# Performance work log

Measured on AMD Instinct MI355X. Metric: run time of the kernel, lower is better.

## Reference

```python
import jax, jax.numpy as jnp
import numpy as np

EPS = 1e-5

def bn_lastdim(x, g, b):
    # BatchNorm2d (training-mode batch stats) applied over all axes except last channel axis
    m = x.mean(axis=(0, 1, 2), keepdims=True)
    v = x.var(axis=(0, 1, 2), keepdims=True)
    return g * (x - m) * jax.lax.rsqrt(v + EPS) + b

def setup_inputs() -> dict:
    key = jax.random.key(0)
    ks = jax.random.split(key, 8)
    B, N, M, F1, K = 8, 8192, 2048, 64, 32
    PF, OUT, DIV = 64, 128, 4
    IN_CH = PF + F1  # 128
    inp = {
        "points": jax.random.normal(ks[0], (B, N, 3), jnp.float32),
        "queries": jax.random.normal(ks[1], (B, M, 3), jnp.float32),
        "feat_prev": jax.random.normal(ks[2], (B, N, F1), jnp.float32),
        # Lift params: linear1 3->32, linear2 32->64
        "w1": jax.random.normal(ks[3], (3, PF // 2), jnp.float32) * 0.1,
        "b1": jnp.zeros((PF // 2,), jnp.float32),
        "w2": jax.random.normal(ks[4], (PF // 2, PF), jnp.float32) * 0.1,
        "b2": jnp.zeros((PF,), jnp.float32),
        # batchnorm affine params (bn1 over 3, bn2 over 32, bn3 over in_channel)
        "g1": jnp.ones((3,), jnp.float32), "be1": jnp.zeros((3,), jnp.float32),
        "g2": jnp.ones((PF // 2,), jnp.float32), "be2": jnp.zeros((PF // 2,), jnp.float32),
        "g3": jnp.ones((IN_CH,), jnp.float32), "be3": jnp.zeros((IN_CH,), jnp.float32),
        # conv2d (out, in, 1, division) -> drop singleton H dim
        "wc": jax.random.normal(ks[5], (OUT, IN_CH, DIV), jnp.float32) * 0.05,
        "bc": jnp.zeros((OUT,), jnp.float32),
    }
    return inp

def reference(points, queries, feat_prev, w1, b1, w2, b2, g1, be1, g2, be2, g3, be3, wc, bc):
    K = 32
    DIV = 4
    S = K // DIV  # maxpool window/stride along neighbor axis
    B = points.shape[0]

    # ---- KNN: squared distances (same ordering as torch.cdist + topk smallest) ----
    pn = jnp.sum(points * points, axis=-1)   # (B,N)
    qn = jnp.sum(queries * queries, axis=-1) # (B,M)
    d2 = qn[:, :, None] + pn[:, None, :] - 2.0 * jnp.einsum('bmd,bnd->bmn', queries, points)
    _, idx = jax.lax.top_k(-d2, K)           # idx: (B,M,K), sorted nearest-first

    batch_ix = jnp.arange(B)[:, None, None]
    knn_pts = points[batch_ix, idx]          # (B,M,K,3)
    local = queries[:, :, None, :] - knn_pts # (B,M,K,3)

    # ---- Lift MLP (with batchnorm, training-mode stats) ----
    h = bn_lastdim(local, g1, be1)
    h = jax.nn.relu(h @ w1 + b1)             # (B,M,K,32)
    h = bn_lastdim(h, g2, be2)
    h = jax.nn.relu(h @ w2 + b2)             # (B,M,K,64)

    # ---- gather previous features, concat ----
    knn_prev = feat_prev[batch_ix, idx]      # (B,M,K,F1)
    feat = jnp.concatenate([h, knn_prev], axis=-1)  # (B,M,K,C) C=128

    # ---- maxpool over neighbor axis (window S, stride S) ----
    Bq, M, _, C = feat.shape
    feat = feat.reshape(Bq, M, DIV, S, C).max(axis=3)  # (B,M,DIV,C)

    # ---- BN + conv2d kernel (1,DIV) + relu; width collapses to 1 ----
    feat = bn_lastdim(feat, g3, be3)
    out = jnp.einsum('bmdc,ocd->bmo', feat, wc) + bc
    return jax.nn.relu(out)                  # (B,M,out_features)
```

## Files before the change

kernel.cpp:

```cpp
#include <hip/hip_runtime.h>
#include <math.h>

#define B_   8
#define N_   8192
#define M_   2048
#define KNN  32
#define F1_  64
#define HID  32
#define DIV_ 4

typedef unsigned long long u64;
typedef unsigned int u32;

__global__ __launch_bounds__(256) void pack_kernel(
    const float* __restrict__ points, float4* __restrict__ ppk)
{
  const int i = blockIdx.x*256 + threadIdx.x;
  const float* pp = &points[(size_t)i*3];
  float px = pp[0], py = pp[1], pz = pp[2];
  float pn = __builtin_fmaf(pz, pz, __builtin_fmaf(py, py, __fmul_rn(px, px)));
  ppk[i] = make_float4(px, py, pz, pn);
}

__device__ __forceinline__ u32 ord_f32(float f) {
  u32 u = __float_as_uint(f);
  return u ^ (u32)(((int)u >> 31) | 0x80000000);
}

#define KNN_INSERT(PV, NV)                                                    \
  {                                                                           \
    const u32 n_ = (NV);                                                      \
    _Pragma("unroll")                                                         \
    for (int q = 0; q < 2; ++q) {                                             \
      float dot = __builtin_fmaf(qz[q], (PV).z,                               \
                  __builtin_fmaf(qy[q], (PV).y, __fmul_rn(qx[q], (PV).x)));   \
      float s_  = __fadd_rn(qn[q], (PV).w);                                   \
      float d2  = __builtin_fmaf(-2.0f, dot, s_);                             \
      const bool lt0 = d2 < c0[q];                                            \
      const bool lt1 = d2 < c1[q];                                            \
      const bool lt2 = d2 < c2[q];                                            \
      c2[q] = lt1 ? c1[q] : (lt2 ? d2 : c2[q]);                               \
      i2[q] = lt1 ? i1[q] : (lt2 ? n_ : i2[q]);                               \
      c1[q] = lt0 ? c0[q] : (lt1 ? d2 : c1[q]);                               \
      i1[q] = lt0 ? i0[q] : (lt1 ? n_ : i1[q]);                               \
      c0[q] = lt0 ? d2 : c0[q];                                               \
      i0[q] = lt0 ? n_ : i0[q];                                               \
    }                                                                         \
  }

__global__ __launch_bounds__(256, 6) void knn_kernel(
    const float4* __restrict__ ppk, const float* __restrict__ queries,
    int* __restrict__ idx_out, float* __restrict__ local_out)
{
  const int bid = blockIdx.x;
  const int b = bid >> 8;
  const int qbase = (bid & 255) * 8;
  const int t = threadIdx.x, lane = t & 63, wid = t >> 6;

  const int q0 = qbase + wid*2;
  float qx[2], qy[2], qz[2], qn[2];
  float c0[2], c1[2], c2[2];
  u32 i0[2], i1[2], i2[2];
  #pragma unroll
  for (int q = 0; q < 2; ++q) {
    int m = q0 + q;
    qx[q] = queries[(b*M_+m)*3+0];
    qy[q] = queries[(b*M_+m)*3+1];
    qz[q] = queries[(b*M_+m)*3+2];
    qn[q] = __builtin_fmaf(qz[q], qz[q], __builtin_fmaf(qy[q], qy[q], __fmul_rn(qx[q], qx[q])));
    c0[q] = c1[q] = c2[q] = __builtin_inff();
    i0[q] = i1[q] = i2[q] = 0u;
  }

  const float4* __restrict__ base = ppk + (size_t)b * N_;

  float4 pa = base[lane];
  float4 pb = base[64 + lane];
  #pragma unroll 2
  for (int j = 0; j < 126; ++j) {
    const float4 pc = base[(j+2)*64 + lane];
    KNN_INSERT(pa, j*64 + lane);
    pa = pb; pb = pc;
  }
  KNN_INSERT(pa, 126*64 + lane);
  KNN_INSERT(pb, 127*64 + lane);

  u64 e0[2], e1[2], e2[2];
  #pragma unroll
  for (int q = 0; q < 2; ++q) {
    e0[q] = ((u64)ord_f32(c0[q]) << 32) | i0[q];
    e1[q] = ((u64)ord_f32(c1[q]) << 32) | i1[q];
    e2[q] = ((u64)ord_f32(c2[q]) << 32) | i2[q];
  }
  u64 cand[2] = {e0[0], e0[1]};
  u64 mykey[2] = {~0ull, ~0ull};
  int rem[2] = {3, 3};

  for (int r = 0; r < KNN; ++r) {
    u64 wa = cand[0], wb = cand[1];
    #pragma unroll
    for (int dlt = 1; dlt < 64; dlt <<= 1) {
      u64 oa = __shfl_xor(wa, dlt);
      u64 ob = __shfl_xor(wb, dlt);
      wa = oa < wa ? oa : wa;
      wb = ob < wb ? ob : wb;
    }
    if (lane == r) { mykey[0] = wa; mykey[1] = wb; }
    u64 w2q[2] = {wa, wb};
    #pragma unroll
    for (int q = 0; q < 2; ++q) {
      const u64 w = w2q[q];
      if (cand[q] == w) {
        e0[q] = e1[q]; e1[q] = e2[q]; e2[q] = ~0ull; --rem[q];
        if (rem[q] == 0) {
          const u64 lim = w;
          u64 f0 = ~0ull, f1 = ~0ull, f2 = ~0ull;
          for (int j = 0; j < 128; ++j) {
            int n = j*64 + lane;
            const float4 p = base[n];
            float dot = __builtin_fmaf(qz[q], p.z, __builtin_fmaf(qy[q], p.y, __fmul_rn(qx[q], p.x)));
            float d2  = __builtin_fmaf(-2.0f, dot, __fadd_rn(qn[q], p.w));
            u64 key = ((u64)ord_f32(d2) << 32) | (u32)n;
            if (key > lim) {
              u64 a0 = key < f0 ? key : f0;
              u64 A0 = key < f0 ? f0  : key;
              u64 a1 = A0 < f1 ? A0   : f1;
              u64 A1 = A0 < f1 ? f1   : A0;
              u64 a2 = A1 < f2 ? A1   : f2;
              f0 = a0; f1 = a1; f2 = a2;
            }
          }
          e0[q] = f0; e1[q] = f1; e2[q] = f2;
          rem[q] = (f2 != ~0ull) ? 3 : ((f1 != ~0ull) ? 2 : ((f0 != ~0ull) ? 1 : 0));
        }
        cand[q] = e0[q];
      }
    }
  }

  #pragma unroll
  for (int q = 0; q < 2; ++q) {
    if (lane < KNN) {
      u32 n = (u32)mykey[q];
      int bm = b*M_ + q0 + q;
      idx_out[bm*KNN + lane] = (int)n;
      const float4 p = base[n];
      local_out[(bm*KNN + lane)*3 + 0] = qx[q] - p.x;
      local_out[(bm*KNN + lane)*3 + 1] = qy[q] - p.y;
      local_out[(bm*KNN + lane)*3 + 2] = qz[q] - p.z;
    }
  }
}

__global__ __launch_bounds__(256) void bn1_stats_kernel(
    const float* __restrict__ local, float* __restrict__ p1)
{
  const int t = threadIdx.x;
  const int gid = blockIdx.x*256 + t;
  float s0=0,s1=0,s2=0,q0=0,q1=0,q2=0;
  for (int r = gid; r < B_*M_*KNN; r += 65536) {
    float a = local[r*3+0], b = local[r*3+1], c = local[r*3+2];
    s0 += a; s1 += b; s2 += c;
    q0 = fmaf(a,a,q0); q1 = fmaf(b,b,q1); q2 = fmaf(c,c,q2);
  }
  __shared__ float red[256][8];
  red[t][0]=s0; red[t][1]=s1; red[t][2]=s2; red[t][3]=0.f;
  red[t][4]=q0; red[t][5]=q1; red[t][6]=q2; red[t][7]=0.f;
  __syncthreads();
  for (int st = 128; st >= 1; st >>= 1) {
    if (t < st) {
      #pragma unroll
      for (int j = 0; j < 8; ++j) red[t][j] += red[t+st][j];
    }
    __syncthreads();
  }
  if (t < 8) p1[blockIdx.x*8 + t] = red[0][t];
}

__global__ __launch_bounds__(128) void bn1_fold_kernel(
    const float* __restrict__ p1, const float* __restrict__ g1, const float* __restrict__ be1,
    const float* __restrict__ w1, const float* __restrict__ b1, float* __restrict__ prm)
{
  __shared__ float sc[3], sh[3];
  const int t = threadIdx.x;
  if (t < 3) {
    double s = 0, q = 0;
    for (int blk = 0; blk < 256; ++blk) { s += p1[blk*8+t]; q += p1[blk*8+4+t]; }
    double n = (double)(B_*M_*KNN);
    double m = s/n, v = q/n - m*m;
    double rs = 1.0/sqrt(v + 1e-5);
    float scale = (float)((double)g1[t]*rs);
    sc[t] = scale; sh[t] = be1[t] - (float)m*scale;
  }
  __syncthreads();
  if (t < 96) prm[t] = w1[t]*sc[t/32];
  if (t < 32) {
    float a = b1[t];
    for (int c = 0; c < 3; ++c) a = fmaf(sh[c], w1[c*32+t], a);
    prm[96+t] = a;
  }
}

__global__ __launch_bounds__(256) void h1_stats_kernel(
    const float* __restrict__ local, const float* __restrict__ prm, float* __restrict__ p2)
{
  const int t = threadIdx.x;
  const int k4 = (t & 7) * 4;
  float w0[4], w1q[4], w2q[4], b1q[4];
  #pragma unroll
  for (int i = 0; i < 4; ++i) {
    w0[i]  = prm[ 0 + k4 + i];
    w1q[i] = prm[32 + k4 + i];
    w2q[i] = prm[64 + k4 + i];
    b1q[i] = prm[96 + k4 + i];
  }
  float s[4] = {0,0,0,0}, sq[4] = {0,0,0,0};
  const int r0 = (blockIdx.x*256 + t) >> 3;
  for (int r = r0; r < B_*M_*KNN; r += 16384) {
    float l0 = local[r*3+0], l1 = local[r*3+1], l2 = local[r*3+2];
    #pragma unroll
    for (int i = 0; i < 4; ++i) {
      float v = fmaf(l2, w2q[i], fmaf(l1, w1q[i], fmaf(l0, w0[i], b1q[i])));
      v = fmaxf(v, 0.0f);
      s[i] += v; sq[i] = fmaf(v, v, sq[i]);
    }
  }
  __shared__ float red[256][8];
  #pragma unroll
  for (int i = 0; i < 4; ++i) { red[t][i] = s[i]; red[t][4+i] = sq[i]; }
  __syncthreads();
  for (int st = 128; st >= 8; st >>= 1) {
    if (t < st) {
      #pragma unroll
      for (int j = 0; j < 8; ++j) red[t][j] += red[t+st][j];
    }
    __syncthreads();
  }
  if (t < 8) {
    #pragma unroll
    for (int i = 0; i < 4; ++i) {
      p2[blockIdx.x*64 +      t*4 + i] = red[t][i];
      p2[blockIdx.x*64 + 32 + t*4 + i] = red[t][4+i];
    }
  }
}

__global__ __launch_bounds__(64) void bn2_fold_kernel(
    const float* __restrict__ p2, const float* __restrict__ g2, const float* __restrict__ be2,
    const float* __restrict__ w2, const float* __restrict__ b2, float* __restrict__ prm)
{
  __shared__ float sc[32], sh[32];
  const int t = threadIdx.x;
  if (t < 32) {
    double s = 0, q = 0;
    for (int blk = 0; blk < 512; ++blk) { s += p2[blk*64+t]; q += p2[blk*64+32+t]; }
    double n = (double)(B_*M_*KNN);
    double m = s/n, v = q/n - m*m;
    double rs = 1.0/sqrt(v + 1e-5);
    float scale = (float)((double)g2[t]*rs);
    sc[t] = scale; sh[t] = be2[t] - (float)m*scale;
  }
  __syncthreads();
  {
    int j = t;
    float a = b2[j];
    for (int k = 0; k < 32; ++k) {
      float wv = w2[k*64 + j];
      prm[128 + j*32 + k] = wv * sc[k];
      a = fmaf(sh[k], wv, a);
    }
    prm[2176 + j] = a;
  }
}

__global__ __launch_bounds__(256) void h2_prev_pool_kernel(
    const float* __restrict__ local, const float* __restrict__ prm,
    const float* __restrict__ feat_prev, const int* __restrict__ idx,
    float* __restrict__ pooled)
{
  const int t = threadIdx.x;
  const int row = blockIdx.x*256 + t;
  const int bm = row >> 5, s = row & 31, d = s >> 3;
  const float l0 = local[row*3+0], l1 = local[row*3+1], l2 = local[row*3+2];
  float h1v[32];
  #pragma unroll
  for (int k = 0; k < 32; ++k) {
    float v = fmaf(l2, prm[64+k], fmaf(l1, prm[32+k], fmaf(l0, prm[0+k], prm[96+k])));
    h1v[k] = fmaxf(v, 0.0f);
  }
  const float* __restrict__ w2t = prm + 128;
  const float* __restrict__ b2f = prm + 2176;
  #pragma unroll 4
  for (int j = 0; j < 64; ++j) {
    float acc = b2f[j];
    #pragma unroll
    for (int k = 0; k < 32; ++k) acc = fmaf(h1v[k], w2t[j*32+k], acc);
    acc = fmaxf(acc, 0.0f);
    acc = fmaxf(acc, __shfl_xor(acc, 1));
    acc = fmaxf(acc, __shfl_xor(acc, 2));
    acc = fmaxf(acc, __shfl_xor(acc, 4));
    if ((s & 7) == 0) pooled[(bm*4 + d)*128 + j] = acc;
  }
  const int bm0 = blockIdx.x * 8;
  #pragma unroll
  for (int it = 0; it < 8; ++it) {
    const int task = it*256 + t;
    const int bmL  = task >> 8;
    const int dd   = (task >> 6) & 3;
    const int ch   = task & 63;
    const int bmg  = bm0 + bmL;
    const int bb   = bmg >> 11;
    float pm = -3.402823466e+38f;
    #pragma unroll
    for (int s8 = 0; s8 < 8; ++s8) {
      int n = idx[bmg*KNN + dd*8 + s8];
      float v = feat_prev[((size_t)(bb*N_ + n))*64 + ch];
      pm = fmaxf(pm, v);
    }
    pooled[(size_t)(bmg*4 + dd)*128 + 64 + ch] = pm;
  }
}

__global__ __launch_bounds__(256) void bn3_stats_kernel(
    const float* __restrict__ pooled, float* __restrict__ p3)
{
  const int t = threadIdx.x, c = t & 127, rr = t >> 7;
  float s = 0, q = 0;
  for (int r = blockIdx.x*2 + rr; r < B_*M_*DIV_; r += 512) {
    float v = pooled[(size_t)r*128 + c];
    s += v; q = fmaf(v, v, q);
  }
  __shared__ float red[256][2];
  red[t][0] = s; red[t][1] = q;
  __syncthreads();
  if (t < 128) {
    p3[blockIdx.x*256 +       t] = red[t][0] + red[t+128][0];
    p3[blockIdx.x*256 + 128 + t] = red[t][1] + red[t+128][1];
  }
}

__global__ __launch_bounds__(256) void bn3_fold_kernel(
    const float* __restrict__ p3, const float* __restrict__ g3, const float* __restrict__ be3,
    const float* __restrict__ wc, const float* __restrict__ bc, float* __restrict__ prm)
{
  __shared__ float sc[128], sh[128];
  const int t = threadIdx.x;
  if (t < 128) {
    double s = 0, q = 0;
    for (int blk = 0; blk < 256; ++blk) { s += p3[blk*256+t]; q += p3[blk*256+128+t]; }
    double n = (double)(B_*M_*DIV_);
    double m = s/n, v = q/n - m*m;
    double rs = 1.0/sqrt(v + 1e-5);
    float scale = (float)((double)g3[t]*rs);
    sc[t] = scale; sh[t] = be3[t] - (float)m*scale;
  }
  __syncthreads();
  for (int e = t; e < 512*128; e += 256) {
    int i = e >> 7, o = e & 127, dd = i >> 7, cc = i & 127;
    prm[2240 + e] = wc[o*512 + cc*4 + dd] * sc[cc];
  }
  if (t < 128) {
    int o = t;
    float a = bc[o];
    for (int cc = 0; cc < 128; ++cc) {
      float hsum = 0;
      #pragma unroll
      for (int dd = 0; dd < 4; ++dd) hsum += wc[o*512 + cc*4 + dd];
      a = fmaf(sh[cc], hsum, a);
    }
    prm[67776 + o] = a;
  }
}

__global__ __launch_bounds__(256) void conv_gemm_kernel(
    const float* __restrict__ pooled, const float* __restrict__ prm,
    float* __restrict__ outp)
{
  const float* __restrict__ Bw  = prm + 2240;
  const float* __restrict__ bcf = prm + 67776;
  __shared__ float As[32][36];
  __shared__ float Bs[32][128];
  const int t = threadIdx.x;
  const int cg_ = t & 15, rg = t >> 4;
  const int rowbase = blockIdx.x * 32;
  float acc[2][8];
  #pragma unroll
  for (int i = 0; i < 2; ++i)
    #pragma unroll
    for (int j = 0; j < 8; ++j) acc[i][j] = 0.f;

  float bb[8];
  #pragma unroll
  for (int j = 0; j < 8; ++j) bb[j] = bcf[cg_*8 + j];

  for (int k0 = 0; k0 < 512; k0 += 32) {
    {
      int r = t >> 3, qd = t & 7;
      const float4 v = *(const float4*)&pooled[(size_t)(rowbase+r)*512 + k0 + qd*4];
      As[qd*4+0][r] = v.x; As[qd*4+1][r] = v.y; As[qd*4+2][r] = v.z; As[qd*4+3][r] = v.w;
    }
    #pragma unroll
    for (int i = 0; i < 4; ++i) {
      int li = t + i*256;
      int kk = li >> 5, c4 = (li & 31) * 4;
      *(float4*)&Bs[kk][c4] = *(const float4*)&Bw[(size_t)(k0+kk)*128 + c4];
    }
    __syncthreads();
    #pragma unroll 8
    for (int kk = 0; kk < 32; ++kk) {
      float a0 = As[kk][rg*2], a1 = As[kk][rg*2+1];
      float4 b0 = *(const float4*)&Bs[kk][cg_*8];
      float4 b1 = *(const float4*)&Bs[kk][cg_*8+4];
      float bv[8] = {b0.x, b0.y, b0.z, b0.w, b1.x, b1.y, b1.z, b1.w};
      #pragma unroll
      for (int j = 0; j < 8; ++j) {
        acc[0][j] = fmaf(a0, bv[j], acc[0][j]);
        acc[1][j] = fmaf(a1, bv[j], acc[1][j]);
      }
    }
    __syncthreads();
  }
  #pragma unroll
  for (int i = 0; i < 2; ++i) {
    int r = rowbase + rg*2 + i;
    float4 o0, o1;
    o0.x = fmaxf(acc[i][0] + bb[0], 0.f);
    o0.y = fmaxf(acc[i][1] + bb[1], 0.f);
    o0.z = fmaxf(acc[i][2] + bb[2], 0.f);
    o0.w = fmaxf(acc[i][3] + bb[3], 0.f);
    o1.x = fmaxf(acc[i][4] + bb[4], 0.f);
    o1.y = fmaxf(acc[i][5] + bb[5], 0.f);
    o1.z = fmaxf(acc[i][6] + bb[6], 0.f);
    o1.w = fmaxf(acc[i][7] + bb[7], 0.f);
    *(float4*)&outp[(size_t)r*128 + cg_*8    ] = o0;
    *(float4*)&outp[(size_t)r*128 + cg_*8 + 4] = o1;
  }
}

extern "C" void kernel_launch(void* const* d_in, const int* in_sizes, int n_in,
                              void* d_out, int out_size, void* d_ws, size_t ws_size,
                              hipStream_t stream)
{
  (void)in_sizes; (void)n_in; (void)out_size; (void)ws_size;
  const float* points    = (const float*)d_in[0];
  const float* queries   = (const float*)d_in[1];
  const float* feat_prev = (const float*)d_in[2];
  const float* w1  = (const float*)d_in[3];
  const float* b1  = (const float*)d_in[4];
  const float* w2  = (const float*)d_in[5];
  const float* b2  = (const float*)d_in[6];
  const float* g1  = (const float*)d_in[7];
  const float* be1 = (const float*)d_in[8];
  const float* g2  = (const float*)d_in[9];
  const float* be2 = (const float*)d_in[10];
  const float* g3  = (const float*)d_in[11];
  const float* be3 = (const float*)d_in[12];
  const float* wc  = (const float*)d_in[13];
  const float* bc  = (const float*)d_in[14];
  float* outp = (float*)d_out;

  char* ws = (char*)d_ws;
  int*   idx    = (int*)ws;
  float* local  = (float*)(ws + (2u<<20));
  float* pooled = (float*)(ws + (8u<<20));
  float* prm    = (float*)(ws + (40u<<20));
  float* p1     = (float*)(ws + (41u<<20));
  float* p2     = p1 + 8192;
  float4* ppk   = (float4*)(ws + (42u<<20));
  float* p3     = (float*)(ws + (43u<<20));

  pack_kernel    <<<256,   256, 0, stream>>>(points, ppk);
  knn_kernel     <<<2048,  256, 0, stream>>>(ppk, queries, idx, local);
  bn1_stats_kernel<<<256,  256, 0, stream>>>(local, p1);
  bn1_fold_kernel<<<1,     128, 0, stream>>>(p1, g1, be1, w1, b1, prm);
  h1_stats_kernel<<<512,   256, 0, stream>>>(local, prm, p2);
  bn2_fold_kernel<<<1,      64, 0, stream>>>(p2, g2, be2, w2, b2, prm);
  h2_prev_pool_kernel<<<2048, 256, 0, stream>>>(local, prm, feat_prev, idx, pooled);
  bn3_stats_kernel<<<256,  256, 0, stream>>>(pooled, p3);
  bn3_fold_kernel<<<1,     256, 0, stream>>>(p3, g3, be3, wc, bc, prm);
  conv_gemm_kernel<<<512,  256, 0, stream>>>(pooled, prm, outp);
}
```

Baseline: 560.5 us.

## Fuse BN1 and BN3 statistic reductions into producer kernels

Computes per-block BN1 partial sums inside the KNN kernel epilogue and BN3 partial sums at the end of the pooling kernel, dropping two separate stats kernels that re-read local and pooled from memory. The fold kernels now reduce 2048 per-block partials instead of 256, and the p2 offset moves to make room. This removes two launches and a full re-read of the pooled buffer, but adds a block-wide shared-memory reduction and syncs to the KNN kernel and a longer serial reduction in the single-block fold kernels.

```diff
diff --git a/kernel.cpp b/kernel.cpp
--- a/kernel.cpp
+++ b/kernel.cpp
@@ -50,7 +50,8 @@
 
 __global__ __launch_bounds__(256, 6) void knn_kernel(
     const float4* __restrict__ ppk, const float* __restrict__ queries,
-    int* __restrict__ idx_out, float* __restrict__ local_out)
+    int* __restrict__ idx_out, float* __restrict__ local_out,
+    float* __restrict__ p1)
 {
   const int bid = blockIdx.x;
   const int b = bid >> 8;
@@ -138,6 +139,7 @@
     }
   }
 
+  float lx[2] = {0.f, 0.f}, ly[2] = {0.f, 0.f}, lz[2] = {0.f, 0.f};
   #pragma unroll
   for (int q = 0; q < 2; ++q) {
     if (lane < KNN) {
@@ -145,27 +147,22 @@
       int bm = b*M_ + q0 + q;
       idx_out[bm*KNN + lane] = (int)n;
       const float4 p = base[n];
-      local_out[(bm*KNN + lane)*3 + 0] = qx[q] - p.x;
-      local_out[(bm*KNN + lane)*3 + 1] = qy[q] - p.y;
-      local_out[(bm*KNN + lane)*3 + 2] = qz[q] - p.z;
-    }
-  }
-}
-
-__global__ __launch_bounds__(256) void bn1_stats_kernel(
-    const float* __restrict__ local, float* __restrict__ p1)
-{
-  const int t = threadIdx.x;
-  const int gid = blockIdx.x*256 + t;
-  float s0=0,s1=0,s2=0,q0=0,q1=0,q2=0;
-  for (int r = gid; r < B_*M_*KNN; r += 65536) {
-    float a = local[r*3+0], b = local[r*3+1], c = local[r*3+2];
-    s0 += a; s1 += b; s2 += c;
-    q0 = fmaf(a,a,q0); q1 = fmaf(b,b,q1); q2 = fmaf(c,c,q2);
-  }
+      lx[q] = qx[q] - p.x;
+      ly[q] = qy[q] - p.y;
+      lz[q] = qz[q] - p.z;
+      local_out[(bm*KNN + lane)*3 + 0] = lx[q];
+      local_out[(bm*KNN + lane)*3 + 1] = ly[q];
+      local_out[(bm*KNN + lane)*3 + 2] = lz[q];
+    }
+  }
+
   __shared__ float red[256][8];
+  float s0 = lx[0] + lx[1], s1 = ly[0] + ly[1], s2 = lz[0] + lz[1];
+  float v0 = fmaf(lx[0],lx[0], lx[1]*lx[1]);
+  float v1 = fmaf(ly[0],ly[0], ly[1]*ly[1]);
+  float v2 = fmaf(lz[0],lz[0], lz[1]*lz[1]);
   red[t][0]=s0; red[t][1]=s1; red[t][2]=s2; red[t][3]=0.f;
-  red[t][4]=q0; red[t][5]=q1; red[t][6]=q2; red[t][7]=0.f;
+  red[t][4]=v0; red[t][5]=v1; red[t][6]=v2; red[t][7]=0.f;
   __syncthreads();
   for (int st = 128; st >= 1; st >>= 1) {
     if (t < st) {
@@ -174,18 +171,26 @@
     }
     __syncthreads();
   }
-  if (t < 8) p1[blockIdx.x*8 + t] = red[0][t];
+  if (t < 8) p1[bid*8 + t] = red[0][t];
 }
 
 __global__ __launch_bounds__(128) void bn1_fold_kernel(
     const float* __restrict__ p1, const float* __restrict__ g1, const float* __restrict__ be1,
     const float* __restrict__ w1, const float* __restrict__ b1, float* __restrict__ prm)
 {
+  __shared__ double sred[8][16];
   __shared__ float sc[3], sh[3];
   const int t = threadIdx.x;
+  {
+    const int slot = t & 7, grp = t >> 3;
+    double acc = 0;
+    for (int blk = grp; blk < 2048; blk += 16) acc += (double)p1[blk*8 + slot];
+    sred[slot][grp] = acc;
+  }
+  __syncthreads();
   if (t < 3) {
     double s = 0, q = 0;
-    for (int blk = 0; blk < 256; ++blk) { s += p1[blk*8+t]; q += p1[blk*8+4+t]; }
+    for (int g = 0; g < 16; ++g) { s += sred[t][g]; q += sred[4+t][g]; }
     double n = (double)(B_*M_*KNN);
     double m = s/n, v = q/n - m*m;
     double rs = 1.0/sqrt(v + 1e-5);
@@ -276,7 +281,7 @@
 __global__ __launch_bounds__(256) void h2_prev_pool_kernel(
     const float* __restrict__ local, const float* __restrict__ prm,
     const float* __restrict__ feat_prev, const int* __restrict__ idx,
-    float* __restrict__ pooled)
+    float* __restrict__ pooled, float* __restrict__ p3)
 {
   const int t = threadIdx.x;
   const int row = blockIdx.x*256 + t;
@@ -319,19 +324,18 @@
     }
     pooled[(size_t)(bmg*4 + dd)*128 + 64 + ch] = pm;
   }
-}
-
-__global__ __launch_bounds__(256) void bn3_stats_kernel(
-    const float* __restrict__ pooled, float* __restrict__ p3)
-{
-  const int t = threadIdx.x, c = t & 127, rr = t >> 7;
-  float s = 0, q = 0;
-  for (int r = blockIdx.x*2 + rr; r < B_*M_*DIV_; r += 512) {
-    float v = pooled[(size_t)r*128 + c];
-    s += v; q = fmaf(v, v, q);
+
+  __syncthreads();
+  const int ch = t & 127, rr = t >> 7;
+  const int rbase = blockIdx.x * 32;
+  float ps = 0.f, pq = 0.f;
+  #pragma unroll 4
+  for (int r = rr; r < 32; r += 2) {
+    float v = pooled[(size_t)(rbase + r)*128 + ch];
+    ps += v; pq = fmaf(v, v, pq);
   }
   __shared__ float red[256][2];
-  red[t][0] = s; red[t][1] = q;
+  red[t][0] = ps; red[t][1] = pq;
   __syncthreads();
   if (t < 128) {
     p3[blockIdx.x*256 +       t] = red[t][0] + red[t+128][0];
@@ -345,16 +349,22 @@
 {
   __shared__ float sc[128], sh[128];
   const int t = threadIdx.x;
-  if (t < 128) {
-    double s = 0, q = 0;
-    for (int blk = 0; blk < 256; ++blk) { s += p3[blk*256+t]; q += p3[blk*256+128+t]; }
-    double n = (double)(B_*M_*DIV_);
-    double m = s/n, v = q/n - m*m;
-    double rs = 1.0/sqrt(v + 1e-5);
-    float scale = (float)((double)g3[t]*rs);
-    sc[t] = scale; sh[t] = be3[t] - (float)m*scale;
-  }
-  __syncthreads();
+  {
+    const int c = t & 127, half = t >> 7;
+    double acc = 0;
+    for (int blk = 0; blk < 2048; ++blk) acc += (double)p3[blk*256 + half*128 + c];
+    __shared__ double dred[2][128];
+    dred[half][c] = acc;
+    __syncthreads();
+    if (t < 128) {
+      double n = (double)(B_*M_*DIV_);
+      double m = dred[0][t]/n, v = dred[1][t]/n - m*m;
+      double rs = 1.0/sqrt(v + 1e-5);
+      float scale = (float)((double)g3[t]*rs);
+      sc[t] = scale; sh[t] = be3[t] - (float)m*scale;
+    }
+    __syncthreads();
+  }
   for (int e = t; e < 512*128; e += 256) {
     int i = e >> 7, o = e & 127, dd = i >> 7, cc = i & 127;
     prm[2240 + e] = wc[o*512 + cc*4 + dd] * sc[cc];
@@ -465,18 +475,16 @@
   float* pooled = (float*)(ws + (8u<<20));
   float* prm    = (float*)(ws + (40u<<20));
   float* p1     = (float*)(ws + (41u<<20));
-  float* p2     = p1 + 8192;
+  float* p2     = p1 + 16384;
   float4* ppk   = (float4*)(ws + (42u<<20));
   float* p3     = (float*)(ws + (43u<<20));
 
   pack_kernel    <<<256,   256, 0, stream>>>(points, ppk);
-  knn_kernel     <<<2048,  256, 0, stream>>>(ppk, queries, idx, local);
-  bn1_stats_kernel<<<256,  256, 0, stream>>>(local, p1);
+  knn_kernel     <<<2048,  256, 0, stream>>>(ppk, queries, idx, local, p1);
   bn1_fold_kernel<<<1,     128, 0, stream>>>(p1, g1, be1, w1, b1, prm);
   h1_stats_kernel<<<512,   256, 0, stream>>>(local, prm, p2);
   bn2_fold_kernel<<<1,      64, 0, stream>>>(p2, g2, be2, w2, b2, prm);
-  h2_prev_pool_kernel<<<2048, 256, 0, stream>>>(local, prm, feat_prev, idx, pooled);
-  bn3_stats_kernel<<<256,  256, 0, stream>>>(pooled, p3);
+  h2_prev_pool_kernel<<<2048, 256, 0, stream>>>(local, prm, feat_prev, idx, pooled, p3);
   bn3_fold_kernel<<<1,     256, 0, stream>>>(p3, g3, be3, wc, bc, prm);
   conv_gemm_kernel<<<512,  256, 0, stream>>>(pooled, prm, outp);
 }
```

Result: slower. 592.1 us (+5.6%).
